# Kernel tuning notes

Hardware: AMD Instinct MI355X
Metric: run time of the kernel (lower is better)

## Reference

```python
import jax, jax.numpy as jnp
import numpy as np

H = 96  # LSTM units hardcoded in the module


def setup_inputs() -> dict:
    key = jax.random.key(0)
    ks = jax.random.split(key, 5)
    B, LAT, V = 32, 64, 10000
    z = jax.random.normal(ks[0], (B, LAT), dtype=jnp.float32)
    # Keras LSTM params: kernel [in,4H], recurrent_kernel [H,4H], bias [4H]; gate order i,f,c,o
    W = jax.random.normal(ks[1], (LAT, 4 * H), dtype=jnp.float32) * 0.05
    U = jax.random.normal(ks[2], (H, 4 * H), dtype=jnp.float32) * 0.05
    b = jnp.zeros((4 * H,), dtype=jnp.float32)
    Wd = jax.random.normal(ks[3], (H, V), dtype=jnp.float32) * 0.05
    bd = jnp.zeros((V,), dtype=jnp.float32)
    return {"z": z, "W": W, "U": U, "b": b, "Wd": Wd, "bd": bd, "seq_len": 512}


def reference(z, W, U, b, Wd, bd, seq_len):
    # RepeatVector: every timestep sees the same input z, so the input
    # projection z@W + b is computed once and reused across all T steps.
    zp = z @ W + b  # [B, 4H]
    B = z.shape[0]
    h0 = jnp.zeros((B, H), z.dtype)
    c0 = jnp.zeros((B, H), z.dtype)

    def step(carry, _):
        h, c = carry
        g = zp + h @ U  # [B, 4H]
        i = jax.nn.sigmoid(g[:, :H])
        f = jax.nn.sigmoid(g[:, H:2 * H])
        cbar = jnp.tanh(g[:, 2 * H:3 * H])
        o = jax.nn.sigmoid(g[:, 3 * H:])
        c = f * c + i * cbar
        h = o * jnp.tanh(c)
        return (h, c), h

    _, hs = jax.lax.scan(step, (h0, c0), None, length=seq_len)  # [T, B, H]
    hs = jnp.transpose(hs, (1, 0, 2))  # [B, T, H]
    logits = hs @ Wd + bd  # [B, T, V]
    return jax.nn.softmax(logits, axis=-1)
```

## Files before the change

kernel.cpp:

```cpp
#include <hip/hip_runtime.h>
#include <cmath>

#define B_SZ  32
#define LATD  64
#define HU    96
#define G4    384
#define T_LEN 512
#define VOC   10000
#define NROWS (B_SZ * T_LEN)
#define NC16  625
#define NSPLIT 5
#define C16S  125
#define RBLK  32
#define PPR   (NSPLIT * 2)
#define PACK_BLOCKS ((NC16 * 3 * 64 + 383) / 384)
#define LSTM_GRID   (B_SZ + PACK_BLOCKS)

typedef __attribute__((ext_vector_type(8))) short bf16x8;
typedef __attribute__((ext_vector_type(4))) float f32x4;

__device__ __forceinline__ unsigned short f2bf(float x) {
  unsigned u = __float_as_uint(x);
  u += 0x7fffu + ((u >> 16) & 1u);
  return (unsigned short)(u >> 16);
}
__device__ __forceinline__ float fsig(float x) {
  return __builtin_amdgcn_rcpf(1.f + __expf(-x));
}
__device__ __forceinline__ float ftanh(float x) {
  return 1.f - 2.f * __builtin_amdgcn_rcpf(1.f + __expf(2.f * x));
}

__global__ __launch_bounds__(384) void lstm_fused(
    const float* __restrict__ z, const float* __restrict__ W,
    const float* __restrict__ U, const float* __restrict__ bias,
    const float* __restrict__ Wd, unsigned short* __restrict__ hsb,
    uint4* __restrict__ Bp) {
  const int tid = threadIdx.x;

  if (blockIdx.x >= B_SZ) {
    const int gid = (blockIdx.x - B_SZ) * 384 + tid;
    if (gid < NC16 * 3 * 64) {
      const int l   = gid & 63;
      const int K16 = (gid >> 6) % 3;
      const int c16 = gid / 192;
      const int col = c16 * 16 + (l & 15);
      const int k0  = K16 * 32 + (l >> 4) * 8;
      unsigned wb[4];
#pragma unroll
      for (int jj = 0; jj < 4; ++jj) {
        float x0 = Wd[(size_t)(k0 + 2 * jj) * VOC + col];
        float x1 = Wd[(size_t)(k0 + 2 * jj + 1) * VOC + col];
        wb[jj] = (unsigned)f2bf(x0) | ((unsigned)f2bf(x1) << 16);
      }
      Bp[gid] = make_uint4(wb[0], wb[1], wb[2], wb[3]);
    }
    return;
  }

  __shared__ __align__(16) unsigned short hbuf[2][HU];
  __shared__ float z_lds[LATD];
  const int bb = blockIdx.x;
  const int l  = tid & 63, wv = tid >> 6;
  const int c  = l & 15, kg = l >> 4, k0 = kg * 8;

  if (tid < LATD)   z_lds[tid] = z[bb * LATD + tid];
  if (tid < HU / 2) ((unsigned*)hbuf[0])[tid] = 0u;

  int cols[4];
#pragma unroll
  for (int g = 0; g < 4; ++g) cols[g] = (6 * g + wv) * 16 + c;

  bf16x8 Ufr[4][3];
#pragma unroll
  for (int g = 0; g < 4; ++g) {
#pragma unroll
    for (int kt = 0; kt < 3; ++kt) {
      const int kb = kt * 32 + k0;
      unsigned wb[4];
#pragma unroll
      for (int jj = 0; jj < 4; ++jj) {
        float x0 = U[(size_t)(kb + 2 * jj) * G4 + cols[g]];
        float x1 = U[(size_t)(kb + 2 * jj + 1) * G4 + cols[g]];
        wb[jj] = (unsigned)f2bf(x0) | ((unsigned)f2bf(x1) << 16);
      }
      uint4 u4 = make_uint4(wb[0], wb[1], wb[2], wb[3]);
      Ufr[g][kt] = __builtin_bit_cast(bf16x8, u4);
    }
  }

  float zp[4];
#pragma unroll
  for (int g = 0; g < 4; ++g) zp[g] = bias[cols[g]];
  __syncthreads();
  for (int k = 0; k < LATD; ++k) {
    const float zk = z_lds[k];
    const float* wr = W + (size_t)k * G4;
#pragma unroll
    for (int g = 0; g < 4; ++g) zp[g] = fmaf(zk, wr[cols[g]], zp[g]);
  }

  float cst = 0.f;
  unsigned short* hrow = hsb + (size_t)bb * T_LEN * HU;
  int p = 0;
  const f32x4 zero4 = {0.f, 0.f, 0.f, 0.f};

  for (int s = 0; s < T_LEN; ++s) {
    bf16x8 afr[3];
#pragma unroll
    for (int kt = 0; kt < 3; ++kt)
      afr[kt] = *(const bf16x8*)(&hbuf[p][kt * 32 + k0]);

    float g4[4];
#pragma unroll
    for (int g = 0; g < 4; ++g) {
      f32x4 d = __builtin_amdgcn_mfma_f32_16x16x32_bf16(afr[0], Ufr[g][0], zero4, 0, 0, 0);
      d = __builtin_amdgcn_mfma_f32_16x16x32_bf16(afr[1], Ufr[g][1], d, 0, 0, 0);
      d = __builtin_amdgcn_mfma_f32_16x16x32_bf16(afr[2], Ufr[g][2], d, 0, 0, 0);
      g4[g] = d[0] + zp[g];
    }

    const float i_ = fsig(g4[0]);
    const float f_ = fsig(g4[1]);
    const float cb = ftanh(g4[2]);
    const float o_ = fsig(g4[3]);
    cst = f_ * cst + i_ * cb;
    const float h = o_ * ftanh(cst);
    const unsigned short hb = f2bf(h);
    if (kg == 0)      hbuf[p ^ 1][c + 16 * wv] = hb;
    else if (kg == 1) hrow[(size_t)s * HU + c + 16 * wv] = hb;
    __syncthreads();
    p ^= 1;
  }
}

template <int PASS>
__global__ __launch_bounds__(256) void dense_pass(
    const unsigned short* __restrict__ hsb, const bf16x8* __restrict__ Bp,
    const float* __restrict__ bd, const float* __restrict__ invS,
    float* __restrict__ outp) {
  __shared__ __align__(16) unsigned short Al[RBLK * HU];
  const int tid = threadIdx.x;
  const int l = tid & 63, wv = tid >> 6;
  const int r16 = wv & 1, cg = wv >> 1;
  const int l15 = l & 15, l4 = l >> 4;
  const int s = blockIdx.x / 512, rb = blockIdx.x % 512;
  const int R0 = rb * RBLK;

  {
    const uint4* src = (const uint4*)(hsb + (size_t)R0 * HU);
    uint4* dst = (uint4*)Al;
    for (int i = tid; i < RBLK * HU / 8; i += 256) dst[i] = src[i];
  }
  __syncthreads();

  bf16x8 afr[3];
#pragma unroll
  for (int K16 = 0; K16 < 3; ++K16)
    afr[K16] = *(const bf16x8*)(Al + (r16 * 16 + l15) * HU + K16 * 32 + l4 * 8);

  float iv[4];
  float ssum[4] = {0.f, 0.f, 0.f, 0.f};
  if (PASS == 1) {
#pragma unroll
    for (int q = 0; q < 4; ++q) iv[q] = invS[R0 + r16 * 16 + l4 * 4 + q];
  }

  const int cbase = s * C16S;
  for (int i = cg; i < C16S; i += 2) {
    const int c16 = cbase + i;
    const bf16x8* bp = Bp + (size_t)c16 * 192 + l;
    const bf16x8 b0 = bp[0], b1 = bp[64], b2 = bp[128];
    f32x4 acc = {0.f, 0.f, 0.f, 0.f};
    acc = __builtin_amdgcn_mfma_f32_16x16x32_bf16(afr[0], b0, acc, 0, 0, 0);
    acc = __builtin_amdgcn_mfma_f32_16x16x32_bf16(afr[1], b1, acc, 0, 0, 0);
    acc = __builtin_amdgcn_mfma_f32_16x16x32_bf16(afr[2], b2, acc, 0, 0, 0);
    const int col = c16 * 16 + l15;
    const float bdv = bd[col];
    if (PASS == 0) {
#pragma unroll
      for (int q = 0; q < 4; ++q) ssum[q] += __expf(acc[q] + bdv);
    } else {
#pragma unroll
      for (int q = 0; q < 4; ++q) {
        const size_t r = (size_t)(R0 + r16 * 16 + l4 * 4 + q);
        __builtin_nontemporal_store(__expf(acc[q] + bdv) * iv[q],
                                    outp + r * VOC + col);
      }
    }
  }

  if (PASS == 0) {
#pragma unroll
    for (int q = 0; q < 4; ++q) {
      float v = ssum[q];
      v += __shfl_xor(v, 1);
      v += __shfl_xor(v, 2);
      v += __shfl_xor(v, 4);
      v += __shfl_xor(v, 8);
      ssum[q] = v;
    }
    if (l15 == 0) {
#pragma unroll
      for (int q = 0; q < 4; ++q)
        outp[(size_t)(R0 + r16 * 16 + l4 * 4 + q) * PPR + s * 2 + cg] = ssum[q];
    }
  }
}

__global__ __launch_bounds__(256) void reduce_inv(const float* __restrict__ part,
                                                  float* __restrict__ invS) {
  const int r = blockIdx.x * 256 + threadIdx.x;
  if (r < NROWS) {
    float s = 0.f;
#pragma unroll
    for (int i = 0; i < PPR; ++i) s += part[(size_t)r * PPR + i];
    invS[r] = 1.f / s;
  }
}

extern "C" void kernel_launch(void* const* d_in, const int* in_sizes, int n_in,
                              void* d_out, int out_size, void* d_ws, size_t ws_size,
                              hipStream_t stream) {
  const float* z  = (const float*)d_in[0];
  const float* W  = (const float*)d_in[1];
  const float* U  = (const float*)d_in[2];
  const float* b  = (const float*)d_in[3];
  const float* Wd = (const float*)d_in[4];
  const float* bd = (const float*)d_in[5];
  float* out = (float*)d_out;

  char* ws = (char*)d_ws;
  unsigned short* hsb = (unsigned short*)ws;
  uint4* Bp   = (uint4*)(ws + 3145728);
  float* part = (float*)(ws + 3145728 + 1920000);
  float* invS = (float*)(ws + 3145728 + 1920000 + 655360);

  lstm_fused<<<LSTM_GRID, 384, 0, stream>>>(z, W, U, b, Wd, hsb, Bp);
  dense_pass<0><<<512 * NSPLIT, 256, 0, stream>>>(hsb, (const bf16x8*)Bp, bd,
                                                  nullptr, part);
  reduce_inv<<<(NROWS + 255) / 256, 256, 0, stream>>>(part, invS);
  dense_pass<1><<<512 * NSPLIT, 256, 0, stream>>>(hsb, (const bf16x8*)Bp, bd,
                                                  invS, out);
}
```

Baseline: 507.1 us.

## Halve LSTM block size, transpose dense MFMA for vector stores, fold reduce kernel

The LSTM recurrence now runs with 192 threads per block, each lane computing two hidden units. Each gate's three-step MFMA chain is split into two independent partial accumulations to shorten the dependency chain. The dense pass swaps MFMA operands so every lane holds four consecutive columns of one row, which allows 16-byte nontemporal stores and vector bias loads. The separate reduce_inv kernel is removed: pass 1 sums the row partials itself and computes the reciprocal, saving a launch at the cost of redundant partial reads in every block.

```diff
diff --git a/kernel.cpp b/kernel.cpp
--- a/kernel.cpp
+++ b/kernel.cpp
@@ -13,7 +13,7 @@
 #define C16S  125
 #define RBLK  32
 #define PPR   (NSPLIT * 2)
-#define PACK_BLOCKS ((NC16 * 3 * 64 + 383) / 384)
+#define PACK_BLOCKS ((NC16 * 3 * 64) / 192)
 #define LSTM_GRID   (B_SZ + PACK_BLOCKS)
 
 typedef __attribute__((ext_vector_type(8))) short bf16x8;
@@ -31,7 +31,7 @@
   return 1.f - 2.f * __builtin_amdgcn_rcpf(1.f + __expf(2.f * x));
 }
 
-__global__ __launch_bounds__(384) void lstm_fused(
+__global__ __launch_bounds__(192) void lstm_fused(
     const float* __restrict__ z, const float* __restrict__ W,
     const float* __restrict__ U, const float* __restrict__ bias,
     const float* __restrict__ Wd, unsigned short* __restrict__ hsb,
@@ -39,22 +39,20 @@
   const int tid = threadIdx.x;
 
   if (blockIdx.x >= B_SZ) {
-    const int gid = (blockIdx.x - B_SZ) * 384 + tid;
-    if (gid < NC16 * 3 * 64) {
-      const int l   = gid & 63;
-      const int K16 = (gid >> 6) % 3;
-      const int c16 = gid / 192;
-      const int col = c16 * 16 + (l & 15);
-      const int k0  = K16 * 32 + (l >> 4) * 8;
-      unsigned wb[4];
-#pragma unroll
-      for (int jj = 0; jj < 4; ++jj) {
-        float x0 = Wd[(size_t)(k0 + 2 * jj) * VOC + col];
-        float x1 = Wd[(size_t)(k0 + 2 * jj + 1) * VOC + col];
-        wb[jj] = (unsigned)f2bf(x0) | ((unsigned)f2bf(x1) << 16);
-      }
-      Bp[gid] = make_uint4(wb[0], wb[1], wb[2], wb[3]);
+    const int gid = (blockIdx.x - B_SZ) * 192 + tid;
+    const int l   = gid & 63;
+    const int K16 = (gid >> 6) % 3;
+    const int c16 = gid / 192;
+    const int col = c16 * 16 + (l & 15);
+    const int k0  = K16 * 32 + (l >> 4) * 8;
+    unsigned wb[4];
+#pragma unroll
+    for (int jj = 0; jj < 4; ++jj) {
+      float x0 = Wd[(size_t)(k0 + 2 * jj) * VOC + col];
+      float x1 = Wd[(size_t)(k0 + 2 * jj + 1) * VOC + col];
+      wb[jj] = (unsigned)f2bf(x0) | ((unsigned)f2bf(x1) << 16);
     }
+    Bp[gid] = make_uint4(wb[0], wb[1], wb[2], wb[3]);
     return;
   }
 
@@ -67,43 +65,51 @@
   if (tid < LATD)   z_lds[tid] = z[bb * LATD + tid];
   if (tid < HU / 2) ((unsigned*)hbuf[0])[tid] = 0u;
 
-  int cols[4];
-#pragma unroll
-  for (int g = 0; g < 4; ++g) cols[g] = (6 * g + wv) * 16 + c;
-
-  bf16x8 Ufr[4][3];
-#pragma unroll
-  for (int g = 0; g < 4; ++g) {
-#pragma unroll
-    for (int kt = 0; kt < 3; ++kt) {
-      const int kb = kt * 32 + k0;
-      unsigned wb[4];
-#pragma unroll
-      for (int jj = 0; jj < 4; ++jj) {
-        float x0 = U[(size_t)(kb + 2 * jj) * G4 + cols[g]];
-        float x1 = U[(size_t)(kb + 2 * jj + 1) * G4 + cols[g]];
-        wb[jj] = (unsigned)f2bf(x0) | ((unsigned)f2bf(x1) << 16);
+  int cols[2][4];
+#pragma unroll
+  for (int u = 0; u < 2; ++u)
+#pragma unroll
+    for (int g = 0; g < 4; ++g) cols[u][g] = (6 * g + wv + 3 * u) * 16 + c;
+
+  bf16x8 Ufr[2][4][3];
+#pragma unroll
+  for (int u = 0; u < 2; ++u)
+#pragma unroll
+    for (int g = 0; g < 4; ++g)
+#pragma unroll
+      for (int kt = 0; kt < 3; ++kt) {
+        const int kb = kt * 32 + k0;
+        unsigned wb[4];
+#pragma unroll
+        for (int jj = 0; jj < 4; ++jj) {
+          float x0 = U[(size_t)(kb + 2 * jj) * G4 + cols[u][g]];
+          float x1 = U[(size_t)(kb + 2 * jj + 1) * G4 + cols[u][g]];
+          wb[jj] = (unsigned)f2bf(x0) | ((unsigned)f2bf(x1) << 16);
+        }
+        uint4 u4 = make_uint4(wb[0], wb[1], wb[2], wb[3]);
+        Ufr[u][g][kt] = __builtin_bit_cast(bf16x8, u4);
       }
-      uint4 u4 = make_uint4(wb[0], wb[1], wb[2], wb[3]);
-      Ufr[g][kt] = __builtin_bit_cast(bf16x8, u4);
-    }
-  }
-
-  float zp[4];
-#pragma unroll
-  for (int g = 0; g < 4; ++g) zp[g] = bias[cols[g]];
+
+  float zp[2][4];
+#pragma unroll
+  for (int u = 0; u < 2; ++u)
+#pragma unroll
+    for (int g = 0; g < 4; ++g) zp[u][g] = bias[cols[u][g]];
   __syncthreads();
   for (int k = 0; k < LATD; ++k) {
     const float zk = z_lds[k];
     const float* wr = W + (size_t)k * G4;
 #pragma unroll
-    for (int g = 0; g < 4; ++g) zp[g] = fmaf(zk, wr[cols[g]], zp[g]);
-  }
-
-  float cst = 0.f;
+    for (int u = 0; u < 2; ++u)
+#pragma unroll
+      for (int g = 0; g < 4; ++g) zp[u][g] = fmaf(zk, wr[cols[u][g]], zp[u][g]);
+  }
+
+  float cst[2] = {0.f, 0.f};
   unsigned short* hrow = hsb + (size_t)bb * T_LEN * HU;
   int p = 0;
   const f32x4 zero4 = {0.f, 0.f, 0.f, 0.f};
+  const int u0 = c + 16 * wv, u1 = u0 + 48;
 
   for (int s = 0; s < T_LEN; ++s) {
     bf16x8 afr[3];
@@ -111,24 +117,31 @@
     for (int kt = 0; kt < 3; ++kt)
       afr[kt] = *(const bf16x8*)(&hbuf[p][kt * 32 + k0]);
 
-    float g4[4];
-#pragma unroll
-    for (int g = 0; g < 4; ++g) {
-      f32x4 d = __builtin_amdgcn_mfma_f32_16x16x32_bf16(afr[0], Ufr[g][0], zero4, 0, 0, 0);
-      d = __builtin_amdgcn_mfma_f32_16x16x32_bf16(afr[1], Ufr[g][1], d, 0, 0, 0);
-      d = __builtin_amdgcn_mfma_f32_16x16x32_bf16(afr[2], Ufr[g][2], d, 0, 0, 0);
-      g4[g] = d[0] + zp[g];
+    float gate[2][4];
+#pragma unroll
+    for (int u = 0; u < 2; ++u)
+#pragma unroll
+      for (int g = 0; g < 4; ++g) {
+        f32x4 da = __builtin_amdgcn_mfma_f32_16x16x32_bf16(afr[0], Ufr[u][g][0], zero4, 0, 0, 0);
+        da = __builtin_amdgcn_mfma_f32_16x16x32_bf16(afr[2], Ufr[u][g][2], da, 0, 0, 0);
+        f32x4 db = __builtin_amdgcn_mfma_f32_16x16x32_bf16(afr[1], Ufr[u][g][1], zero4, 0, 0, 0);
+        gate[u][g] = (da[0] + db[0]) + zp[u][g];
+      }
+
+    unsigned short hb[2];
+#pragma unroll
+    for (int u = 0; u < 2; ++u) {
+      const float i_ = fsig(gate[u][0]);
+      const float f_ = fsig(gate[u][1]);
+      const float cb = ftanh(gate[u][2]);
+      const float o_ = fsig(gate[u][3]);
+      cst[u] = f_ * cst[u] + i_ * cb;
+      hb[u] = f2bf(o_ * ftanh(cst[u]));
     }
-
-    const float i_ = fsig(g4[0]);
-    const float f_ = fsig(g4[1]);
-    const float cb = ftanh(g4[2]);
-    const float o_ = fsig(g4[3]);
-    cst = f_ * cst + i_ * cb;
-    const float h = o_ * ftanh(cst);
-    const unsigned short hb = f2bf(h);
-    if (kg == 0)      hbuf[p ^ 1][c + 16 * wv] = hb;
-    else if (kg == 1) hrow[(size_t)s * HU + c + 16 * wv] = hb;
+    if (kg == 0)      hbuf[p ^ 1][u0] = hb[0];
+    else if (kg == 3) hbuf[p ^ 1][u1] = hb[1];
+    else if (kg == 1) hrow[(size_t)s * HU + u0] = hb[0];
+    else              hrow[(size_t)s * HU + u1] = hb[1];
     __syncthreads();
     p ^= 1;
   }
@@ -137,12 +150,12 @@
 template <int PASS>
 __global__ __launch_bounds__(256) void dense_pass(
     const unsigned short* __restrict__ hsb, const bf16x8* __restrict__ Bp,
-    const float* __restrict__ bd, const float* __restrict__ invS,
+    const float* __restrict__ bd, const float* __restrict__ part,
     float* __restrict__ outp) {
   __shared__ __align__(16) unsigned short Al[RBLK * HU];
   const int tid = threadIdx.x;
   const int l = tid & 63, wv = tid >> 6;
-  const int r16 = wv & 1, cg = wv >> 1;
+  const int rt = wv & 1, cg = wv >> 1;
   const int l15 = l & 15, l4 = l >> 4;
   const int s = blockIdx.x / 512, rb = blockIdx.x % 512;
   const int R0 = rb * RBLK;
@@ -156,66 +169,45 @@
 
   bf16x8 afr[3];
 #pragma unroll
-  for (int K16 = 0; K16 < 3; ++K16)
-    afr[K16] = *(const bf16x8*)(Al + (r16 * 16 + l15) * HU + K16 * 32 + l4 * 8);
-
-  float iv[4];
-  float ssum[4] = {0.f, 0.f, 0.f, 0.f};
+  for (int kt = 0; kt < 3; ++kt)
+    afr[kt] = *(const bf16x8*)(Al + (rt * 16 + l15) * HU + kt * 32 + l4 * 8);
+
+  const int row = R0 + rt * 16 + l15;
+  float iv = 0.f;
   if (PASS == 1) {
-#pragma unroll
-    for (int q = 0; q < 4; ++q) iv[q] = invS[R0 + r16 * 16 + l4 * 4 + q];
-  }
-
-  const int cbase = s * C16S;
+    float sum = 0.f;
+#pragma unroll
+    for (int i = 0; i < PPR; ++i) sum += part[(size_t)row * PPR + i];
+    iv = 1.f / sum;
+  }
+
+  float srun = 0.f;
   for (int i = cg; i < C16S; i += 2) {
-    const int c16 = cbase + i;
+    const int c16 = s * C16S + i;
     const bf16x8* bp = Bp + (size_t)c16 * 192 + l;
     const bf16x8 b0 = bp[0], b1 = bp[64], b2 = bp[128];
     f32x4 acc = {0.f, 0.f, 0.f, 0.f};
-    acc = __builtin_amdgcn_mfma_f32_16x16x32_bf16(afr[0], b0, acc, 0, 0, 0);
-    acc = __builtin_amdgcn_mfma_f32_16x16x32_bf16(afr[1], b1, acc, 0, 0, 0);
-    acc = __builtin_amdgcn_mfma_f32_16x16x32_bf16(afr[2], b2, acc, 0, 0, 0);
-    const int col = c16 * 16 + l15;
-    const float bdv = bd[col];
+    acc = __builtin_amdgcn_mfma_f32_16x16x32_bf16(b0, afr[0], acc, 0, 0, 0);
+    acc = __builtin_amdgcn_mfma_f32_16x16x32_bf16(b1, afr[1], acc, 0, 0, 0);
+    acc = __builtin_amdgcn_mfma_f32_16x16x32_bf16(b2, afr[2], acc, 0, 0, 0);
+    const int colb = c16 * 16 + l4 * 4;
+    const f32x4 bd4 = *(const f32x4*)(bd + colb);
     if (PASS == 0) {
 #pragma unroll
-      for (int q = 0; q < 4; ++q) ssum[q] += __expf(acc[q] + bdv);
+      for (int q = 0; q < 4; ++q) srun += __expf(acc[q] + bd4[q]);
     } else {
-#pragma unroll
-      for (int q = 0; q < 4; ++q) {
-        const size_t r = (size_t)(R0 + r16 * 16 + l4 * 4 + q);
-        __builtin_nontemporal_store(__expf(acc[q] + bdv) * iv[q],
-                                    outp + r * VOC + col);
-      }
+      f32x4 o;
+#pragma unroll
+      for (int q = 0; q < 4; ++q) o[q] = __expf(acc[q] + bd4[q]) * iv;
+      __builtin_nontemporal_store(o, (f32x4*)(outp + (size_t)row * VOC + colb));
     }
   }
 
   if (PASS == 0) {
-#pragma unroll
-    for (int q = 0; q < 4; ++q) {
-      float v = ssum[q];
-      v += __shfl_xor(v, 1);
-      v += __shfl_xor(v, 2);
-      v += __shfl_xor(v, 4);
-      v += __shfl_xor(v, 8);
-      ssum[q] = v;
-    }
-    if (l15 == 0) {
-#pragma unroll
-      for (int q = 0; q < 4; ++q)
-        outp[(size_t)(R0 + r16 * 16 + l4 * 4 + q) * PPR + s * 2 + cg] = ssum[q];
-    }
-  }
-}
-
-__global__ __launch_bounds__(256) void reduce_inv(const float* __restrict__ part,
-                                                  float* __restrict__ invS) {
-  const int r = blockIdx.x * 256 + threadIdx.x;
-  if (r < NROWS) {
-    float s = 0.f;
-#pragma unroll
-    for (int i = 0; i < PPR; ++i) s += part[(size_t)r * PPR + i];
-    invS[r] = 1.f / s;
+    srun += __shfl_xor(srun, 16);
+    srun += __shfl_xor(srun, 32);
+    if (l4 == 0)
+      ((float*)outp)[(size_t)row * PPR + s * 2 + cg] = srun;
   }
 }
 
@@ -234,12 +226,10 @@
   unsigned short* hsb = (unsigned short*)ws;
   uint4* Bp   = (uint4*)(ws + 3145728);
   float* part = (float*)(ws + 3145728 + 1920000);
-  float* invS = (float*)(ws + 3145728 + 1920000 + 655360);
-
-  lstm_fused<<<LSTM_GRID, 384, 0, stream>>>(z, W, U, b, Wd, hsb, Bp);
+
+  lstm_fused<<<LSTM_GRID, 192, 0, stream>>>(z, W, U, b, Wd, hsb, Bp);
   dense_pass<0><<<512 * NSPLIT, 256, 0, stream>>>(hsb, (const bf16x8*)Bp, bd,
                                                   nullptr, part);
-  reduce_inv<<<(NROWS + 255) / 256, 256, 0, stream>>>(part, invS);
   dense_pass<1><<<512 * NSPLIT, 256, 0, stream>>>(hsb, (const bf16x8*)Bp, bd,
-                                                  invS, out);
-}
+                                                  part, out);
+}
```

New measurement: 611.3 us. 20.6% more time.

## Process two batch rows per LSTM block with LDS history ring and batched writeback

Applied to the files above, without the earlier changes.

Each LSTM block now runs two batch sequences at once, halving the LSTM grid, so the two independent MFMA and activation chains can interleave and hide each other's serial latency. The hidden-state history is kept in a 64-step LDS ring per sequence and flushed to global memory in vectorized chunks every 64 steps, replacing per-step scalar global stores. The three-MFMA dependent chain is also split into two partial accumulators to shorten the dependency depth. Per-block step cost rises because each step does twice the work, and an extra barrier is added at every flush.

```diff
diff --git a/kernel.cpp b/kernel.cpp
--- a/kernel.cpp
+++ b/kernel.cpp
@@ -13,8 +13,10 @@
 #define C16S  125
 #define RBLK  32
 #define PPR   (NSPLIT * 2)
+#define HIST  64
+#define NLSTM (B_SZ / 2)
 #define PACK_BLOCKS ((NC16 * 3 * 64 + 383) / 384)
-#define LSTM_GRID   (B_SZ + PACK_BLOCKS)
+#define LSTM_GRID   (NLSTM + PACK_BLOCKS)
 
 typedef __attribute__((ext_vector_type(8))) short bf16x8;
 typedef __attribute__((ext_vector_type(4))) float f32x4;
@@ -31,15 +33,15 @@
   return 1.f - 2.f * __builtin_amdgcn_rcpf(1.f + __expf(2.f * x));
 }
 
-__global__ __launch_bounds__(384) void lstm_fused(
+__global__ __launch_bounds__(384) void lstm_fused2(
     const float* __restrict__ z, const float* __restrict__ W,
     const float* __restrict__ U, const float* __restrict__ bias,
     const float* __restrict__ Wd, unsigned short* __restrict__ hsb,
     uint4* __restrict__ Bp) {
   const int tid = threadIdx.x;
 
-  if (blockIdx.x >= B_SZ) {
-    const int gid = (blockIdx.x - B_SZ) * 384 + tid;
+  if (blockIdx.x >= NLSTM) {
+    const int gid = (blockIdx.x - NLSTM) * 384 + tid;
     if (gid < NC16 * 3 * 64) {
       const int l   = gid & 63;
       const int K16 = (gid >> 6) % 3;
@@ -58,14 +60,18 @@
     return;
   }
 
-  __shared__ __align__(16) unsigned short hbuf[2][HU];
-  __shared__ float z_lds[LATD];
+  __shared__ __align__(16) unsigned short ringA[HIST][HU];
+  __shared__ __align__(16) unsigned short ringB[HIST][HU];
+  __shared__ float z_lds[2][LATD];
   const int bb = blockIdx.x;
   const int l  = tid & 63, wv = tid >> 6;
   const int c  = l & 15, kg = l >> 4, k0 = kg * 8;
 
-  if (tid < LATD)   z_lds[tid] = z[bb * LATD + tid];
-  if (tid < HU / 2) ((unsigned*)hbuf[0])[tid] = 0u;
+  if (tid < 2 * LATD) ((float*)z_lds)[tid] = z[bb * 2 * LATD + tid];
+  if (tid < 12) {
+    ((uint4*)(ringA[HIST - 1]))[tid] = make_uint4(0u, 0u, 0u, 0u);
+    ((uint4*)(ringB[HIST - 1]))[tid] = make_uint4(0u, 0u, 0u, 0u);
+  }
 
   int cols[4];
 #pragma unroll
@@ -89,48 +95,84 @@
     }
   }
 
-  float zp[4];
-#pragma unroll
-  for (int g = 0; g < 4; ++g) zp[g] = bias[cols[g]];
+  float zpA[4], zpB[4];
+#pragma unroll
+  for (int g = 0; g < 4; ++g) { zpA[g] = bias[cols[g]]; zpB[g] = zpA[g]; }
   __syncthreads();
   for (int k = 0; k < LATD; ++k) {
-    const float zk = z_lds[k];
+    const float zkA = z_lds[0][k], zkB = z_lds[1][k];
     const float* wr = W + (size_t)k * G4;
 #pragma unroll
-    for (int g = 0; g < 4; ++g) zp[g] = fmaf(zk, wr[cols[g]], zp[g]);
-  }
-
-  float cst = 0.f;
-  unsigned short* hrow = hsb + (size_t)bb * T_LEN * HU;
-  int p = 0;
+    for (int g = 0; g < 4; ++g) {
+      const float w_ = wr[cols[g]];
+      zpA[g] = fmaf(zkA, w_, zpA[g]);
+      zpB[g] = fmaf(zkB, w_, zpB[g]);
+    }
+  }
+
+  float cstA = 0.f, cstB = 0.f;
+  unsigned short* hrowA = hsb + (size_t)(2 * bb) * T_LEN * HU;
+  unsigned short* hrowB = hsb + (size_t)(2 * bb + 1) * T_LEN * HU;
   const f32x4 zero4 = {0.f, 0.f, 0.f, 0.f};
+  const int u0 = c + 16 * wv;
 
   for (int s = 0; s < T_LEN; ++s) {
-    bf16x8 afr[3];
-#pragma unroll
-    for (int kt = 0; kt < 3; ++kt)
-      afr[kt] = *(const bf16x8*)(&hbuf[p][kt * 32 + k0]);
-
-    float g4[4];
+    const int rs = (s + HIST - 1) & (HIST - 1);
+    bf16x8 afrA[3], afrB[3];
+#pragma unroll
+    for (int kt = 0; kt < 3; ++kt) {
+      afrA[kt] = *(const bf16x8*)(&ringA[rs][kt * 32 + k0]);
+      afrB[kt] = *(const bf16x8*)(&ringB[rs][kt * 32 + k0]);
+    }
+
+    float gA[4], gB[4];
 #pragma unroll
     for (int g = 0; g < 4; ++g) {
-      f32x4 d = __builtin_amdgcn_mfma_f32_16x16x32_bf16(afr[0], Ufr[g][0], zero4, 0, 0, 0);
-      d = __builtin_amdgcn_mfma_f32_16x16x32_bf16(afr[1], Ufr[g][1], d, 0, 0, 0);
-      d = __builtin_amdgcn_mfma_f32_16x16x32_bf16(afr[2], Ufr[g][2], d, 0, 0, 0);
-      g4[g] = d[0] + zp[g];
-    }
-
-    const float i_ = fsig(g4[0]);
-    const float f_ = fsig(g4[1]);
-    const float cb = ftanh(g4[2]);
-    const float o_ = fsig(g4[3]);
-    cst = f_ * cst + i_ * cb;
-    const float h = o_ * ftanh(cst);
-    const unsigned short hb = f2bf(h);
-    if (kg == 0)      hbuf[p ^ 1][c + 16 * wv] = hb;
-    else if (kg == 1) hrow[(size_t)s * HU + c + 16 * wv] = hb;
+      f32x4 da = __builtin_amdgcn_mfma_f32_16x16x32_bf16(afrA[0], Ufr[g][0], zero4, 0, 0, 0);
+      da = __builtin_amdgcn_mfma_f32_16x16x32_bf16(afrA[2], Ufr[g][2], da, 0, 0, 0);
+      f32x4 db = __builtin_amdgcn_mfma_f32_16x16x32_bf16(afrA[1], Ufr[g][1], zero4, 0, 0, 0);
+      gA[g] = (da[0] + db[0]) + zpA[g];
+    }
+#pragma unroll
+    for (int g = 0; g < 4; ++g) {
+      f32x4 da = __builtin_amdgcn_mfma_f32_16x16x32_bf16(afrB[0], Ufr[g][0], zero4, 0, 0, 0);
+      da = __builtin_amdgcn_mfma_f32_16x16x32_bf16(afrB[2], Ufr[g][2], da, 0, 0, 0);
+      f32x4 db = __builtin_amdgcn_mfma_f32_16x16x32_bf16(afrB[1], Ufr[g][1], zero4, 0, 0, 0);
+      gB[g] = (da[0] + db[0]) + zpB[g];
+    }
+
+    {
+      const float i_ = fsig(gA[0]);
+      const float f_ = fsig(gA[1]);
+      const float cb = ftanh(gA[2]);
+      const float o_ = fsig(gA[3]);
+      cstA = f_ * cstA + i_ * cb;
+      const float h = o_ * ftanh(cstA);
+      if (kg == 0) ringA[s & (HIST - 1)][u0] = f2bf(h);
+    }
+    {
+      const float i_ = fsig(gB[0]);
+      const float f_ = fsig(gB[1]);
+      const float cb = ftanh(gB[2]);
+      const float o_ = fsig(gB[3]);
+      cstB = f_ * cstB + i_ * cb;
+      const float h = o_ * ftanh(cstB);
+      if (kg == 0) ringB[s & (HIST - 1)][u0] = f2bf(h);
+    }
     __syncthreads();
-    p ^= 1;
+
+    if ((s & (HIST - 1)) == (HIST - 1)) {
+      const int s0 = s - (HIST - 1);
+      const uint4* srcA = (const uint4*)ringA;
+      const uint4* srcB = (const uint4*)ringB;
+      uint4* dstA = (uint4*)(hrowA + (size_t)s0 * HU);
+      uint4* dstB = (uint4*)(hrowB + (size_t)s0 * HU);
+      for (int i = tid; i < HIST * HU / 8; i += 384) {
+        dstA[i] = srcA[i];
+        dstB[i] = srcB[i];
+      }
+      __syncthreads();
+    }
   }
 }
 
@@ -236,7 +278,7 @@
   float* part = (float*)(ws + 3145728 + 1920000);
   float* invS = (float*)(ws + 3145728 + 1920000 + 655360);
 
-  lstm_fused<<<LSTM_GRID, 384, 0, stream>>>(z, W, U, b, Wd, hsb, Bp);
+  lstm_fused2<<<LSTM_GRID, 384, 0, stream>>>(z, W, U, b, Wd, hsb, Bp);
   dense_pass<0><<<512 * NSPLIT, 256, 0, stream>>>(hsb, (const bf16x8*)Bp, bd,
                                                   nullptr, part);
   reduce_inv<<<(NROWS + 255) / 256, 256, 0, stream>>>(part, invS);
```

New measurement: 712.6 us. 40.5% more time.
